# Performance work log

Measured on AMD Instinct MI355X. Metric: run time of the kernel, lower is better.

The kernel has to match this reference:

```python
import jax, jax.numpy as jnp
import numpy as np

NUM_HEADS = 8
NUM_GROUPS = 32
EPS = 1e-5
RESCALE = 1.0


def setup_inputs() -> dict:
    key = jax.random.key(0)
    ks = jax.random.split(key, 7)
    b, c, h, w = 16, 512, 32, 32
    return {
        "x": jax.random.normal(ks[0], (b, c, h, w), jnp.float32),
        "norm_w": jax.random.normal(ks[1], (c,), jnp.float32),
        "norm_b": jax.random.normal(ks[2], (c,), jnp.float32),
        "qkv_w": jax.random.normal(ks[3], (3 * c, c), jnp.float32) * (c ** -0.5),
        "qkv_b": jax.random.normal(ks[4], (3 * c,), jnp.float32) * 0.02,
        "proj_w": jax.random.normal(ks[5], (c, c), jnp.float32) * (c ** -0.5),
        "proj_b": jax.random.normal(ks[6], (c,), jnp.float32) * 0.02,
    }


def _group_norm(x, w, b):
    # x: [B, C, L]
    B, C, L = x.shape
    g = x.reshape(B, NUM_GROUPS, (C // NUM_GROUPS) * L)
    mu = jnp.mean(g, axis=-1, keepdims=True)
    var = jnp.var(g, axis=-1, keepdims=True)
    g = (g - mu) * jax.lax.rsqrt(var + EPS)
    return g.reshape(B, C, L) * w[None, :, None] + b[None, :, None]


def reference(x, norm_w, norm_b, qkv_w, qkv_b, proj_w, proj_b):
    b, c, hh, ww = x.shape
    L = hh * ww
    H = NUM_HEADS
    ch = c // H  # head dim

    xr = x.reshape(b, c, L)
    hid = _group_norm(xr, norm_w, norm_b)

    # 1x1 conv1d == matmul over channel dim: [3c, c] @ [b, c, L]
    qkv = jnp.einsum('oc,bcl->bol', qkv_w, hid) + qkv_b[None, :, None]
    # torch: reshape(b*H, 3*ch, L).split(ch) -> per-head contiguous [q|k|v] blocks
    qkv = qkv.reshape(b, H, 3, ch, L)
    q, k, v = qkv[:, :, 0], qkv[:, :, 1], qkv[:, :, 2]  # [b, H, ch, L]

    scale = 1.0 / (ch ** 0.25)
    weight = jnp.einsum('bhct,bhcs->bhts', q * scale, k * scale)
    weight = jax.nn.softmax(weight.astype(jnp.float32), axis=-1).astype(weight.dtype)
    a = jnp.einsum('bhts,bhcs->bhct', weight, v)  # [b, H, ch, L]

    h = a.reshape(b, c, L)
    h = jnp.einsum('oc,bcl->bol', proj_w, h) + proj_b[None, :, None]
    h = h.reshape(b, c, hh, ww)
    return (x + h) / RESCALE
```

## Files before the change

kernel.cpp:

```cpp
#include <hip/hip_runtime.h>
#include <hip/hip_bf16.h>
#include <stdint.h>


using f32x4  = __attribute__((ext_vector_type(4))) float;
using bf16x8 = __attribute__((ext_vector_type(8))) __bf16;
using s8v    = __attribute__((ext_vector_type(8))) short;
using s4v    = __attribute__((ext_vector_type(4))) short;

__device__ __forceinline__ short f2bf(float f){
  union { float f; unsigned u; } c; c.f = f;
  unsigned r = (c.u + 0x7FFFu + ((c.u >> 16) & 1u)) >> 16;
  return (short)r;
}

__device__ __forceinline__ float exp2_fast(float x){
#if __has_builtin(__builtin_amdgcn_exp2f)
  return __builtin_amdgcn_exp2f(x);
#else
  return exp2f(x);
#endif
}

__device__ __forceinline__ void gl_lds16(const void* g, void* l){
  __builtin_amdgcn_global_load_lds((const __attribute__((address_space(1))) void*)g,
                                   (__attribute__((address_space(3))) void*)l, 16, 0, 0);
}

__global__ __launch_bounds__(256) void k_pre(const float* __restrict__ x,
                                             const float* __restrict__ w,
                                             const float* __restrict__ bia,
                                             short* __restrict__ hid,
                                             const float* __restrict__ qw,
                                             const float* __restrict__ pw,
                                             const float* __restrict__ qb,
                                             short* __restrict__ qwb,
                                             short* __restrict__ pwb,
                                             float* __restrict__ qbp){
  int bid = blockIdx.x;
  int tid = threadIdx.x;
  if (bid >= 512){
    int i = (bid - 512) * 256 + tid;
    if (i < 786432){
      int o = i >> 9, kk = i & 511;
      int h = o / 192, rem = o - h*192;
      int nr = (rem >> 6)*512 + h*64 + (rem & 63);
      qwb[nr*512 + kk] = f2bf(qw[i]);
    } else if (i < 1048576){
      int j = i - 786432;
      pwb[j] = f2bf(pw[j]);
    } else if (i < 1050112){
      int o = i - 1048576;
      int h = o / 192, rem = o - h*192;
      qbp[(rem >> 6)*512 + h*64 + (rem & 63)] = qb[o];
    }
    return;
  }
  int b = bid >> 5;
  int g = bid & 31;
  const float* xg = x + ((size_t)b*512 + g*16)*1024;
  int l0 = tid * 4;
  float v[16][4];
  float s1 = 0.f, s2 = 0.f;
  #pragma unroll
  for (int c = 0; c < 16; c++){
    f32x4 t = *(const f32x4*)(xg + c*1024 + l0);
    #pragma unroll
    for (int j = 0; j < 4; j++){ v[c][j] = t[j]; s1 += t[j]; s2 += t[j]*t[j]; }
  }
  #pragma unroll
  for (int m = 32; m; m >>= 1){ s1 += __shfl_xor(s1, m); s2 += __shfl_xor(s2, m); }
  __shared__ float r1[4], r2[4];
  int wv = tid >> 6, ln = tid & 63;
  if (ln == 0){ r1[wv] = s1; r2[wv] = s2; }
  __syncthreads();
  s1 = r1[0]+r1[1]+r1[2]+r1[3];
  s2 = r2[0]+r2[1]+r2[2]+r2[3];
  float mu = s1 * (1.f/16384.f);
  float var = s2 * (1.f/16384.f) - mu*mu;
  float rs = rsqrtf(var + 1e-5f);
  float ww[16], bb[16];
  #pragma unroll
  for (int c = 0; c < 16; c++){ ww[c] = w[g*16+c]*rs; bb[c] = bia[g*16+c]; }
  #pragma unroll
  for (int j = 0; j < 4; j++){
    short o[16];
    #pragma unroll
    for (int c = 0; c < 16; c++) o[c] = f2bf((v[c][j]-mu)*ww[c] + bb[c]);
    short* dst = hid + ((size_t)(b*1024 + l0 + j))*512 + g*16;
    *(s8v*)dst     = *(s8v*)o;
    *(s8v*)(dst+8) = *(s8v*)(o+8);
  }
}

template<int EPI>
__global__ __launch_bounds__(256) void k_gemm(
    const short* __restrict__ A, const short* __restrict__ Bm,
    const float* __restrict__ bias, const float* __restrict__ xres,
    short* __restrict__ q_t, short* __restrict__ k_t, short* __restrict__ v_t,
    float* __restrict__ outp)
{
  __shared__ short Al[2][128*64];
  __shared__ short Bl[2][128*64];
  int id = blockIdx.x;
  int xcd = id & 7, ix = id >> 3;
  int mt, nt;
  if (EPI == 0){ mt = ix % 12; nt = ix / 12; }
  else         { mt = ix & 3;  nt = ix >> 2; }
  int m0 = mt * 128;
  int n0 = (xcd + 8*nt) * 128;
  int tid = threadIdx.x;
  int lane = tid & 63;
  int wv = tid >> 6;
  int wr = wv >> 1, wc = wv & 1;
  int l15 = lane & 15, g = lane >> 4;
  f32x4 acc[4][4] = {};

  auto STAGE = [&](int db, int t){
    int k0 = t * 64;
    #pragma unroll
    for (int i = 0; i < 8; i++){
      int cc = wv*8 + i;
      if (cc < 16){
        int slot = cc*64 + lane;
        int row = slot >> 3, off = slot & 7;
        gl_lds16(A + (size_t)(m0+row)*512 + k0 + (off ^ (row&7))*8,
                 (char*)Al[db] + cc*1024);
      } else {
        int slot = (cc-16)*64 + lane;
        int row = slot >> 3, off = slot & 7;
        gl_lds16(Bm + (size_t)(n0+row)*512 + k0 + (off ^ (row&7))*8,
                 (char*)Bl[db] + (cc-16)*1024);
      }
    }
  };

  auto COMPUTE = [&](int db){
    #pragma unroll
    for (int kk = 0; kk < 2; kk++){
      bf16x8 af[4], bf[4];
      #pragma unroll
      for (int m = 0; m < 4; m++){
        int row = wr*64 + m*16 + l15;
        int byte = row*128 + (((kk*64) + (g*16)) ^ ((row&7)<<4));
        af[m] = *(const bf16x8*)((char*)Al[db] + byte);
      }
      #pragma unroll
      for (int n = 0; n < 4; n++){
        int row = wc*64 + n*16 + l15;
        int byte = row*128 + (((kk*64) + (g*16)) ^ ((row&7)<<4));
        bf[n] = *(const bf16x8*)((char*)Bl[db] + byte);
      }
      __builtin_amdgcn_s_setprio(1);
      #pragma unroll
      for (int m = 0; m < 4; m++)
        #pragma unroll
        for (int n = 0; n < 4; n++)
          acc[m][n] = __builtin_amdgcn_mfma_f32_16x16x32_bf16(af[m], bf[n], acc[m][n], 0, 0, 0);
      __builtin_amdgcn_s_setprio(0);
    }
  };

  STAGE(0, 0);
  for (int t = 0; t < 8; t++){
    __syncthreads();
    if (t < 7) STAGE((t+1)&1, t+1);
    COMPUTE(t&1);
  }
  __syncthreads();

  if (EPI == 0){
    int sel = m0 >> 9;
    if (sel < 2){
      const float sc = (sel == 0) ? 0.18033688011112042f : 1.0f;
      short* dstb = (sel == 0) ? q_t : k_t;
      #pragma unroll
      for (int m = 0; m < 4; m++){
        int ob = m0 + wr*64 + m*16 + (g<<2);
        int hh = (ob>>6)&7, c0 = ob&63;
        float bs[4];
        #pragma unroll
        for (int r = 0; r < 4; r++) bs[r] = bias[ob+r];
        #pragma unroll
        for (int n = 0; n < 4; n++){
          int nn = n0 + wc*64 + n*16 + l15;
          int bb = nn >> 10, ll = nn & 1023;
          int bh = bb*8 + hh;
          short o4[4];
          #pragma unroll
          for (int r = 0; r < 4; r++) o4[r] = f2bf((acc[m][n][r] + bs[r]) * sc);
          *(s4v*)(dstb + ((size_t)bh*1024 + ll)*64 + c0) = *(s4v*)o4;
        }
      }
    } else {
      short* Sc = (short*)Al;
      #pragma unroll
      for (int m = 0; m < 4; m++){
        int ob = m0 + wr*64 + m*16 + (g<<2);
        int h2 = (ob>>6)&1, cq = (ob>>4)&3;
        float bs[4];
        #pragma unroll
        for (int r = 0; r < 4; r++) bs[r] = bias[ob+r];
        #pragma unroll
        for (int n = 0; n < 4; n++){
          int nn = n0 + wc*64 + n*16 + l15;
          int sl = nn & 63, sreg = (nn>>6)&1;
          int ks2 = sl >> 5, gq = (sl>>2)&3, i2 = (sl&3) + 4*((sl>>4)&1);
          int base = (h2*2 + sreg)*4096 + (((ks2*4+gq)*4 + cq)*16 + (g<<2))*8 + i2;
          #pragma unroll
          for (int r = 0; r < 4; r++)
            Sc[base + r*8] = f2bf(acc[m][n][r] + bs[r]);
        }
      }
      __syncthreads();
      int b0  = n0 >> 10;
      int s64 = (n0 >> 6) & 15;
      int hb  = (m0 - 1024) >> 6;
      #pragma unroll
      for (int it = 0; it < 8; it++){
        int flat = it*2048 + tid*8;
        int h2 = flat >> 13, rem = flat & 8191, sreg = rem >> 12, off = rem & 4095;
        int bh = b0*8 + hb + h2;
        *(s8v*)(v_t + ((size_t)bh*16 + s64 + sreg)*4096 + off) = *(const s8v*)(Sc + flat);
      }
    }
  } else {
    #pragma unroll
    for (int m = 0; m < 4; m++){
      int ob = m0 + wr*64 + m*16 + (g<<2);
      float bs[4];
      #pragma unroll
      for (int r = 0; r < 4; r++) bs[r] = bias[ob+r];
      #pragma unroll
      for (int n = 0; n < 4; n++){
        int nn = n0 + wc*64 + n*16 + l15;
        int bb = nn >> 10, ll = nn & 1023;
        #pragma unroll
        for (int r = 0; r < 4; r++){
          size_t idx = ((size_t)bb*512 + ob + r)*1024 + ll;
          outp[idx] = xres[idx] + acc[m][n][r] + bs[r];
        }
      }
    }
  }
}

__global__ __launch_bounds__(256, 4) void k_attn(
    const short* __restrict__ q_t, const short* __restrict__ k_t,
    const short* __restrict__ v_t, short* __restrict__ a_bt)
{
  __shared__ short Kh[4*2048];
  __shared__ short Vh[4*2048];
  int id = blockIdx.x;
  int xcd = id & 7, ix = id >> 3;
  int bh = xcd*16 + (ix >> 3);
  int qb = ix & 7;
  int bb = bh >> 3, hh = bh & 7;
  int tid = threadIdx.x;
  int lane = tid & 63;
  int wv = tid >> 6;
  int l15 = lane & 15, g = lane >> 4;

  bf16x8 qf[2][2];
  #pragma unroll
  for (int qt = 0; qt < 2; qt++){
    const short* qbase = q_t + ((size_t)bh*1024 + qb*128 + qt*64 + wv*16 + l15)*64 + g*8;
    qf[qt][0] = *(const bf16x8*)(qbase);
    qf[qt][1] = *(const bf16x8*)(qbase + 32);
  }
  asm volatile("" :: "v"(qf[0][0]), "v"(qf[0][1]), "v"(qf[1][0]), "v"(qf[1][1]));

  bf16x8 onesb;
  #pragma unroll
  for (int i = 0; i < 8; i++) onesb[i] = (__bf16)1.0f;

  f32x4 o[2][4] = {};
  f32x4 osum[2] = {};

  auto STAGE = [&](int db, int h){
    int t64 = h >> 1, ks = h & 1;
    #pragma unroll
    for (int i = 0; i < 2; i++){
      int cc = wv*2 + i;
      if (cc < 4){
        int row = cc*8 + (lane>>3), slot = lane & 7;
        gl_lds16(k_t + ((size_t)bh*1024 + h*32 + row)*64 + ((slot ^ (row&7))*8),
                 (char*)Kh + db*4096 + cc*1024);
      } else {
        gl_lds16(v_t + ((size_t)bh*16 + t64)*4096 + ks*2048 + (cc-4)*512 + lane*8,
                 (char*)Vh + db*4096 + (cc-4)*1024);
      }
    }
  };

  auto COMPUTE = [&](int db){
    const char* Kb = (const char*)Kh + db*4096;
    const char* Vb = (const char*)Vh + db*4096;
    f32x4 scl[2][2] = {};
    #pragma unroll
    for (int jl = 0; jl < 2; jl++){
      int row = jl*16 + l15;
      int swz = (row&7)<<4;
      bf16x8 kf0 = *(const bf16x8*)(Kb + row*128 + ((g*16) ^ swz));
      bf16x8 kf1 = *(const bf16x8*)(Kb + row*128 + ((64 + g*16) ^ swz));
      __builtin_amdgcn_s_setprio(1);
      #pragma unroll
      for (int qt = 0; qt < 2; qt++){
        scl[qt][jl] = __builtin_amdgcn_mfma_f32_16x16x32_bf16(kf0, qf[qt][0], scl[qt][jl], 0, 0, 0);
        scl[qt][jl] = __builtin_amdgcn_mfma_f32_16x16x32_bf16(kf1, qf[qt][1], scl[qt][jl], 0, 0, 0);
      }
      __builtin_amdgcn_s_setprio(0);
    }
    bf16x8 pa[2];
    #pragma unroll
    for (int qt = 0; qt < 2; qt++){
      #pragma unroll
      for (int i2 = 0; i2 < 8; i2++)
        pa[qt][i2] = (__bf16)exp2_fast(scl[qt][i2>>2][i2&3]);
      osum[qt] = __builtin_amdgcn_mfma_f32_16x16x32_bf16(pa[qt], onesb, osum[qt], 0, 0, 0);
    }
    #pragma unroll
    for (int jd = 0; jd < 4; jd++){
      bf16x8 vbb = *(const bf16x8*)(Vb + (g*4+jd)*256 + l15*16);
      __builtin_amdgcn_s_setprio(1);
      #pragma unroll
      for (int qt = 0; qt < 2; qt++)
        o[qt][jd] = __builtin_amdgcn_mfma_f32_16x16x32_bf16(pa[qt], vbb, o[qt][jd], 0, 0, 0);
      __builtin_amdgcn_s_setprio(0);
    }
  };

  STAGE(0, 0);
  STAGE(1, 1);
  #pragma unroll 2
  for (int h = 0; h < 30; h++){
    STAGE((h+2)&3, h+2);
    asm volatile("s_waitcnt vmcnt(4)" ::: "memory");
    __builtin_amdgcn_s_barrier();
    __builtin_amdgcn_sched_barrier(0);
    COMPUTE(h&3);
  }
  asm volatile("s_waitcnt vmcnt(2)" ::: "memory");
  __builtin_amdgcn_s_barrier();
  __builtin_amdgcn_sched_barrier(0);
  COMPUTE(2);
  asm volatile("s_waitcnt vmcnt(0)" ::: "memory");
  __builtin_amdgcn_s_barrier();
  __builtin_amdgcn_sched_barrier(0);
  COMPUTE(3);

  #pragma unroll
  for (int qt = 0; qt < 2; qt++){
    #pragma unroll
    for (int r = 0; r < 4; r++){
      float inv = 1.f / osum[qt][r];
      int qrow = qb*128 + qt*64 + wv*16 + g*4 + r;
      #pragma unroll
      for (int jd = 0; jd < 4; jd++)
        a_bt[((size_t)bb*1024 + qrow)*512 + hh*64 + jd*16 + l15] = f2bf(o[qt][jd][r] * inv);
    }
  }
}

extern "C" void kernel_launch(void* const* d_in, const int* in_sizes, int n_in,
                              void* d_out, int out_size, void* d_ws, size_t ws_size,
                              hipStream_t stream){
  const float* x  = (const float*)d_in[0];
  const float* nw = (const float*)d_in[1];
  const float* nb = (const float*)d_in[2];
  const float* qw = (const float*)d_in[3];
  const float* qb = (const float*)d_in[4];
  const float* pw = (const float*)d_in[5];
  const float* pb = (const float*)d_in[6];
  float* outp = (float*)d_out;

  char* ws = (char*)d_ws;
  short* hid  = (short*)(ws);
  short* qwb  = (short*)(ws + 16777216);
  short* pwb  = (short*)(ws + 18350080);
  short* q_t  = (short*)(ws + 18874368);
  short* k_t  = (short*)(ws + 35651584);
  short* v_t  = (short*)(ws + 52428800);
  short* a_bt = hid;
  float* qbp  = (float*)d_out;
  if (ws_size < 69206016) return;

  k_pre<<<4615, 256, 0, stream>>>(x, nw, nb, hid, qw, pw, qb, qwb, pwb, qbp);
  k_gemm<0><<<1536, 256, 0, stream>>>(qwb, hid, qbp, nullptr, q_t, k_t, v_t, nullptr);
  k_attn<<<1024, 256, 0, stream>>>(q_t, k_t, v_t, a_bt);
  k_gemm<1><<<512, 256, 0, stream>>>(pwb, a_bt, pb, x, nullptr, nullptr, nullptr, outp);
}
```

Measured before the change: 119.5 us.

## Split QKV GEMM into dedicated kernel with 256x128 tiles and shallower K stages

The QKV projection gets its own kernel with a 256-row M tile (8x4 MFMA accumulators per wave) and 32-wide K steps over 16 iterations, halving the grid and raising data reuse per block. The V-transpose epilogue is done in two phases through LDS so it fits the smaller staging buffer. The projection GEMM keeps the old 128x128 path. The larger tile doubles accumulator registers, which may lower occupancy, and more, shorter K iterations add barrier overhead.

```diff
diff --git a/kernel.cpp b/kernel.cpp
--- a/kernel.cpp
+++ b/kernel.cpp
@@ -93,20 +93,142 @@
   }
 }
 
-template<int EPI>
-__global__ __launch_bounds__(256) void k_gemm(
+__global__ __launch_bounds__(256) void k_gemmQ(
+    const short* __restrict__ A, const short* __restrict__ Bm,
+    const float* __restrict__ bias,
+    short* __restrict__ q_t, short* __restrict__ k_t, short* __restrict__ v_t)
+{
+  __shared__ short Lds[24576];
+  int id = blockIdx.x;
+  int xcd = id & 7, ix = id >> 3;
+  int mt = ix % 6, nt = ix / 6;
+  int m0 = mt * 256;
+  int n0 = (xcd + 8*nt) * 128;
+  int tid = threadIdx.x;
+  int lane = tid & 63;
+  int wv = tid >> 6;
+  int wr = wv >> 1, wc = wv & 1;
+  int l15 = lane & 15, g = lane >> 4;
+  f32x4 acc[8][4] = {};
+
+  auto STAGE = [&](int db, int t){
+    int k0 = t * 32;
+    #pragma unroll
+    for (int i = 0; i < 6; i++){
+      int cc = wv*6 + i;
+      int row, byteoff;
+      const short* srcb;
+      if (cc < 16){ row = cc*16 + (lane>>2); srcb = A + (size_t)(m0+row)*512; byteoff = cc*1024; }
+      else        { row = (cc-16)*16 + (lane>>2); srcb = Bm + (size_t)(n0+row)*512; byteoff = 16384 + (cc-16)*1024; }
+      int slot = lane & 3;
+      gl_lds16(srcb + k0 + ((slot ^ ((row>>1)&3))*8),
+               (char*)Lds + db*24576 + byteoff);
+    }
+  };
+
+  auto COMPUTE = [&](int db){
+    const char* Ab = (const char*)Lds + db*24576;
+    const char* Bb = Ab + 16384;
+    bf16x8 af[8], bf[4];
+    #pragma unroll
+    for (int m = 0; m < 8; m++){
+      int row = wr*128 + m*16 + l15;
+      af[m] = *(const bf16x8*)(Ab + row*64 + ((g*16) ^ (((row>>1)&3)<<4)));
+    }
+    #pragma unroll
+    for (int n = 0; n < 4; n++){
+      int row = wc*64 + n*16 + l15;
+      bf[n] = *(const bf16x8*)(Bb + row*64 + ((g*16) ^ (((row>>1)&3)<<4)));
+    }
+    __builtin_amdgcn_s_setprio(1);
+    #pragma unroll
+    for (int m = 0; m < 8; m++)
+      #pragma unroll
+      for (int n = 0; n < 4; n++)
+        acc[m][n] = __builtin_amdgcn_mfma_f32_16x16x32_bf16(af[m], bf[n], acc[m][n], 0, 0, 0);
+    __builtin_amdgcn_s_setprio(0);
+  };
+
+  STAGE(0, 0);
+  for (int t = 0; t < 16; t++){
+    __syncthreads();
+    if (t < 15) STAGE((t+1)&1, t+1);
+    COMPUTE(t&1);
+  }
+
+  int sel = m0 >> 9;
+  if (sel < 2){
+    const float sc = (sel == 0) ? 0.18033688011112042f : 1.0f;
+    short* dstb = (sel == 0) ? q_t : k_t;
+    #pragma unroll
+    for (int m = 0; m < 8; m++){
+      int ob = m0 + wr*128 + m*16 + (g<<2);
+      int hh = (ob>>6)&7, c0 = ob&63;
+      float bs[4];
+      #pragma unroll
+      for (int r = 0; r < 4; r++) bs[r] = bias[ob+r];
+      #pragma unroll
+      for (int n = 0; n < 4; n++){
+        int nn = n0 + wc*64 + n*16 + l15;
+        int bb = nn >> 10, ll = nn & 1023;
+        int bh = bb*8 + hh;
+        short o4[4];
+        #pragma unroll
+        for (int r = 0; r < 4; r++) o4[r] = f2bf((acc[m][n][r] + bs[r]) * sc);
+        *(s4v*)(dstb + ((size_t)bh*1024 + ll)*64 + c0) = *(s4v*)o4;
+      }
+    }
+  } else {
+    short* Sc = Lds;
+    int b0  = n0 >> 10;
+    int s64 = (n0 >> 6) & 15;
+    int hb  = (m0 - 1024) >> 6;
+    #pragma unroll
+    for (int ph = 0; ph < 2; ph++){
+      __syncthreads();
+      if (wr == ph){
+        #pragma unroll
+        for (int m = 0; m < 8; m++){
+          int ob = m0 + wr*128 + m*16 + (g<<2);
+          int h2 = (ob>>6)&1, cq = (ob>>4)&3;
+          float bs[4];
+          #pragma unroll
+          for (int r = 0; r < 4; r++) bs[r] = bias[ob+r];
+          #pragma unroll
+          for (int n = 0; n < 4; n++){
+            int nn = n0 + wc*64 + n*16 + l15;
+            int sl = nn & 63, sreg = (nn>>6)&1;
+            int ks2 = sl >> 5, gq = (sl>>2)&3, i2 = (sl&3) + 4*((sl>>4)&1);
+            int base = (h2*2 + sreg)*4096 + (((ks2*4+gq)*4 + cq)*16 + (g<<2))*8 + i2;
+            #pragma unroll
+            for (int r = 0; r < 4; r++)
+              Sc[base + r*8] = f2bf(acc[m][n][r] + bs[r]);
+          }
+        }
+      }
+      __syncthreads();
+      #pragma unroll
+      for (int it = 0; it < 8; it++){
+        int flat = it*2048 + tid*8;
+        int reg = flat >> 12, off = flat & 4095;
+        int h2 = reg >> 1, sreg = reg & 1;
+        int bh = b0*8 + hb + ph*2 + h2;
+        *(s8v*)(v_t + ((size_t)bh*16 + s64 + sreg)*4096 + off) = *(const s8v*)(Sc + flat);
+      }
+    }
+  }
+}
+
+__global__ __launch_bounds__(256) void k_gemmP(
     const short* __restrict__ A, const short* __restrict__ Bm,
     const float* __restrict__ bias, const float* __restrict__ xres,
-    short* __restrict__ q_t, short* __restrict__ k_t, short* __restrict__ v_t,
     float* __restrict__ outp)
 {
   __shared__ short Al[2][128*64];
   __shared__ short Bl[2][128*64];
   int id = blockIdx.x;
   int xcd = id & 7, ix = id >> 3;
-  int mt, nt;
-  if (EPI == 0){ mt = ix % 12; nt = ix / 12; }
-  else         { mt = ix & 3;  nt = ix >> 2; }
+  int mt = ix & 3, nt = ix >> 2;
   int m0 = mt * 128;
   int n0 = (xcd + 8*nt) * 128;
   int tid = threadIdx.x;
@@ -167,79 +289,21 @@
     if (t < 7) STAGE((t+1)&1, t+1);
     COMPUTE(t&1);
   }
-  __syncthreads();
-
-  if (EPI == 0){
-    int sel = m0 >> 9;
-    if (sel < 2){
-      const float sc = (sel == 0) ? 0.18033688011112042f : 1.0f;
-      short* dstb = (sel == 0) ? q_t : k_t;
-      #pragma unroll
-      for (int m = 0; m < 4; m++){
-        int ob = m0 + wr*64 + m*16 + (g<<2);
-        int hh = (ob>>6)&7, c0 = ob&63;
-        float bs[4];
-        #pragma unroll
-        for (int r = 0; r < 4; r++) bs[r] = bias[ob+r];
-        #pragma unroll
-        for (int n = 0; n < 4; n++){
-          int nn = n0 + wc*64 + n*16 + l15;
-          int bb = nn >> 10, ll = nn & 1023;
-          int bh = bb*8 + hh;
-          short o4[4];
-          #pragma unroll
-          for (int r = 0; r < 4; r++) o4[r] = f2bf((acc[m][n][r] + bs[r]) * sc);
-          *(s4v*)(dstb + ((size_t)bh*1024 + ll)*64 + c0) = *(s4v*)o4;
-        }
-      }
-    } else {
-      short* Sc = (short*)Al;
-      #pragma unroll
-      for (int m = 0; m < 4; m++){
-        int ob = m0 + wr*64 + m*16 + (g<<2);
-        int h2 = (ob>>6)&1, cq = (ob>>4)&3;
-        float bs[4];
-        #pragma unroll
-        for (int r = 0; r < 4; r++) bs[r] = bias[ob+r];
-        #pragma unroll
-        for (int n = 0; n < 4; n++){
-          int nn = n0 + wc*64 + n*16 + l15;
-          int sl = nn & 63, sreg = (nn>>6)&1;
-          int ks2 = sl >> 5, gq = (sl>>2)&3, i2 = (sl&3) + 4*((sl>>4)&1);
-          int base = (h2*2 + sreg)*4096 + (((ks2*4+gq)*4 + cq)*16 + (g<<2))*8 + i2;
-          #pragma unroll
-          for (int r = 0; r < 4; r++)
-            Sc[base + r*8] = f2bf(acc[m][n][r] + bs[r]);
-        }
-      }
-      __syncthreads();
-      int b0  = n0 >> 10;
-      int s64 = (n0 >> 6) & 15;
-      int hb  = (m0 - 1024) >> 6;
-      #pragma unroll
-      for (int it = 0; it < 8; it++){
-        int flat = it*2048 + tid*8;
-        int h2 = flat >> 13, rem = flat & 8191, sreg = rem >> 12, off = rem & 4095;
-        int bh = b0*8 + hb + h2;
-        *(s8v*)(v_t + ((size_t)bh*16 + s64 + sreg)*4096 + off) = *(const s8v*)(Sc + flat);
-      }
-    }
-  } else {
-    #pragma unroll
-    for (int m = 0; m < 4; m++){
-      int ob = m0 + wr*64 + m*16 + (g<<2);
-      float bs[4];
-      #pragma unroll
-      for (int r = 0; r < 4; r++) bs[r] = bias[ob+r];
-      #pragma unroll
-      for (int n = 0; n < 4; n++){
-        int nn = n0 + wc*64 + n*16 + l15;
-        int bb = nn >> 10, ll = nn & 1023;
-        #pragma unroll
-        for (int r = 0; r < 4; r++){
-          size_t idx = ((size_t)bb*512 + ob + r)*1024 + ll;
-          outp[idx] = xres[idx] + acc[m][n][r] + bs[r];
-        }
+
+  #pragma unroll
+  for (int m = 0; m < 4; m++){
+    int ob = m0 + wr*64 + m*16 + (g<<2);
+    float bs[4];
+    #pragma unroll
+    for (int r = 0; r < 4; r++) bs[r] = bias[ob+r];
+    #pragma unroll
+    for (int n = 0; n < 4; n++){
+      int nn = n0 + wc*64 + n*16 + l15;
+      int bb = nn >> 10, ll = nn & 1023;
+      #pragma unroll
+      for (int r = 0; r < 4; r++){
+        size_t idx = ((size_t)bb*512 + ob + r)*1024 + ll;
+        outp[idx] = xres[idx] + acc[m][n][r] + bs[r];
       }
     }
   }
@@ -386,7 +450,7 @@
   if (ws_size < 69206016) return;
 
   k_pre<<<4615, 256, 0, stream>>>(x, nw, nb, hid, qw, pw, qb, qwb, pwb, qbp);
-  k_gemm<0><<<1536, 256, 0, stream>>>(qwb, hid, qbp, nullptr, q_t, k_t, v_t, nullptr);
+  k_gemmQ<<<768, 256, 0, stream>>>(qwb, hid, qbp, q_t, k_t, v_t);
   k_attn<<<1024, 256, 0, stream>>>(q_t, k_t, v_t, a_bt);
-  k_gemm<1><<<512, 256, 0, stream>>>(pwb, a_bt, pb, x, nullptr, nullptr, nullptr, outp);
-}
+  k_gemmP<<<512, 256, 0, stream>>>(pwb, a_bt, pb, x, outp);
+}
```

Result: slower. 136.2 us (+13.9%).
